# Performance work log

Measured on AMD Instinct MI355X. Metric: run time of the kernel, lower is better.

The kernel has to match this reference:

```python
import jax, jax.numpy as jnp
import numpy as np

B, S, D, H, HD = 1, 4096, 1024, 16, 64
ROPE_THETA = 10000.0


def setup_inputs() -> dict:
    key = jax.random.key(0)
    ks = jax.random.split(key, 10)
    sc = 0.02
    hidden_states = jax.random.normal(ks[0], (B, S, D), dtype=jnp.float32)
    # sorted continuous timestamps in [0, S) (irregularly sampled time series)
    timestamps = jnp.sort(jax.random.uniform(ks[1], (B, S), dtype=jnp.float32), axis=-1) * S
    Wq = jax.random.normal(ks[2], (D, D), dtype=jnp.float32) * sc
    bq = jax.random.normal(ks[3], (D,), dtype=jnp.float32) * sc
    Wk = jax.random.normal(ks[4], (D, D), dtype=jnp.float32) * sc
    bk = jax.random.normal(ks[5], (D,), dtype=jnp.float32) * sc
    Wv = jax.random.normal(ks[6], (D, D), dtype=jnp.float32) * sc
    bv = jax.random.normal(ks[7], (D,), dtype=jnp.float32) * sc
    Wo = jax.random.normal(ks[8], (D, D), dtype=jnp.float32) * sc
    return dict(hidden_states=hidden_states, timestamps=timestamps,
                Wq=Wq, bq=bq, Wk=Wk, bk=bk, Wv=Wv, bv=bv, Wo=Wo)


def _rotate_half(x):
    x1, x2 = jnp.split(x, 2, axis=-1)
    return jnp.concatenate([-x2, x1], axis=-1)


def _ct_rope(q, k, timestamps):
    # q,k: [b,h,s,hd]; timestamps: [b,s] continuous positions
    inv_freq = 1.0 / (ROPE_THETA ** (jnp.arange(0, HD, 2, dtype=jnp.float32) / HD))
    angles = timestamps[:, None, :, None] * inv_freq  # [b,1,s,hd/2]
    angles = jnp.concatenate([angles, angles], axis=-1)  # [b,1,s,hd]
    cos, sin = jnp.cos(angles), jnp.sin(angles)
    q = q * cos + _rotate_half(q) * sin
    k = k * cos + _rotate_half(k) * sin
    return q, k


def reference(hidden_states, timestamps, Wq, bq, Wk, bk, Wv, bv, Wo):
    b, s, _ = hidden_states.shape
    # nn.Linear convention: y = x @ W.T + b
    q = (hidden_states @ Wq.T + bq).reshape(b, s, H, HD).transpose(0, 2, 1, 3)
    k = (hidden_states @ Wk.T + bk).reshape(b, s, H, HD).transpose(0, 2, 1, 3)
    v = (hidden_states @ Wv.T + bv).reshape(b, s, H, HD).transpose(0, 2, 1, 3)
    q, k = _ct_rope(q, k, timestamps)
    scores = jnp.einsum('bhqd,bhkd->bhqk', q, k) / jnp.sqrt(jnp.float32(HD))
    # causal additive mask (built as in HF Qwen2Model)
    causal = jnp.tril(jnp.ones((s, s), dtype=bool))
    neg = jnp.finfo(jnp.float32).min
    scores = jnp.where(causal[None, None], scores, neg)
    attn = jax.nn.softmax(scores.astype(jnp.float32), axis=-1).astype(q.dtype)
    out = jnp.einsum('bhqk,bhkd->bhqd', attn, v)
    out = out.transpose(0, 2, 1, 3).reshape(b, s, H * HD)
    return out @ Wo.T
```

## Files before the change

### kernel.cpp

```cpp
#include <hip/hip_runtime.h>

#define S_LEN  4096
#define DMODEL 1024
#define NHEAD  16
#define HDIM   64

typedef float    f32x4  __attribute__((ext_vector_type(4)));
typedef float    f32x16 __attribute__((ext_vector_type(16)));
typedef _Float16 f16x8  __attribute__((ext_vector_type(8)));
typedef _Float16 f16x4v __attribute__((ext_vector_type(4)));
typedef __fp16   fp16x2 __attribute__((ext_vector_type(2)));
typedef unsigned int u32;
typedef u32 u32x4 __attribute__((ext_vector_type(4)));

__device__ __forceinline__ void gl2lds16(const _Float16* g, _Float16* l) {
  __builtin_amdgcn_global_load_lds(
      (const __attribute__((address_space(1))) unsigned int*)g,
      (__attribute__((address_space(3))) unsigned int*)l, 16, 0, 0);
}

__device__ __forceinline__ u32 pkrtz_u(float a, float b) {
  fp16x2 h = __builtin_amdgcn_cvt_pkrtz(a, b);
  return __builtin_bit_cast(u32, h);
}

__device__ __forceinline__ float m3(float a, float b, float c) {
  return fmaxf(fmaxf(a, b), c);
}

__device__ __forceinline__ float ex2(float x) { return __builtin_amdgcn_exp2f(x); }
__device__ __forceinline__ float lg2(float x) { return __builtin_amdgcn_logf(x); }
__device__ __forceinline__ float rcp(float x) { return __builtin_amdgcn_rcpf(x); }

__global__ void cast_all_k(const float* __restrict__ hs,
                           const float* __restrict__ a, const float* __restrict__ b,
                           const float* __restrict__ c, const float* __restrict__ d,
                           _Float16* __restrict__ ohs,
                           _Float16* __restrict__ oa, _Float16* __restrict__ ob,
                           _Float16* __restrict__ oc, _Float16* __restrict__ od) {
  const int bid = blockIdx.x;
  const float* in;
  _Float16* out;
  int local;
  if (bid < 4096) {
    in = hs; out = ohs; local = bid;
  } else {
    const int seg = (bid - 4096) >> 10;
    local = (bid - 4096) & 1023;
    in  = seg == 0 ? a  : seg == 1 ? b  : seg == 2 ? c  : d;
    out = seg == 0 ? oa : seg == 1 ? ob : seg == 2 ? oc : od;
  }
  const int i = (local * 256 + threadIdx.x) * 4;
  const float4 v = *(const float4*)(in + i);
  f16x4v o = { (_Float16)v.x, (_Float16)v.y, (_Float16)v.z, (_Float16)v.w };
  *(f16x4v*)(out + i) = o;
}

__global__ __launch_bounds__(256)
void gemm_qkv(const _Float16* __restrict__ A,
              const _Float16* __restrict__ Bw,
              const float* __restrict__ bq,
              const float* __restrict__ bk,
              const float* __restrict__ bv,
              const float* __restrict__ ts,
              _Float16* __restrict__ Qb,
              _Float16* __restrict__ Kb,
              _Float16* __restrict__ Vtb)
{
  __shared__ _Float16 lA[128 * 64];
  __shared__ _Float16 lB[128 * 64];

  const int tid  = threadIdx.x;
  const int wid  = tid >> 6;
  const int lane = tid & 63;
  const int l16  = lane & 15;
  const int lg   = lane >> 4;
  const int wr = wid >> 1, wc = wid & 1;
  const int bid = blockIdx.x, xcd = bid & 7, ci = bid >> 3;
  const int n0 = (xcd * 3 + ci / 32) * 128;
  const int m0 = (ci & 31) * 128;
  const int K = DMODEL, M = S_LEN;

  const int lrow   = lane >> 3;
  const int gchunk = (lane & 7) ^ lrow;

  f32x4 acc[4][4] = {};

  for (int k0 = 0; k0 < K; k0 += 64) {
#pragma unroll
    for (int it = 0; it < 4; ++it) {
      const int rbase = (it * 4 + wid) * 8;
      gl2lds16(A  + (size_t)(m0 + rbase + lrow) * K + k0 + gchunk * 8, &lA[rbase * 64]);
      gl2lds16(Bw + (size_t)(n0 + rbase + lrow) * K + k0 + gchunk * 8, &lB[rbase * 64]);
    }
    __syncthreads();
#pragma unroll
    for (int kk = 0; kk < 2; ++kk) {
      f16x8 af[4], bfr[4];
#pragma unroll
      for (int mr = 0; mr < 4; ++mr) {
        const int row = wr * 64 + mr * 16 + l16;
        const int ch  = (kk * 4 + lg) ^ (l16 & 7);
        af[mr] = *(const f16x8*)&lA[row * 64 + ch * 8];
      }
#pragma unroll
      for (int nr = 0; nr < 4; ++nr) {
        const int row = wc * 64 + nr * 16 + l16;
        const int ch  = (kk * 4 + lg) ^ (l16 & 7);
        bfr[nr] = *(const f16x8*)&lB[row * 64 + ch * 8];
      }
#pragma unroll
      for (int mr = 0; mr < 4; ++mr)
#pragma unroll
        for (int nr = 0; nr < 4; ++nr)
          acc[mr][nr] = __builtin_amdgcn_mfma_f32_16x16x32_f16(af[mr], bfr[nr], acc[mr][nr], 0, 0, 0);
    }
    __syncthreads();
  }

  if (n0 >= 2048) {
    const int dbase = n0 - 2048;
    float bvv[4];
#pragma unroll
    for (int nr = 0; nr < 4; ++nr) bvv[nr] = bv[dbase + wc * 64 + nr * 16 + l16];
#pragma unroll
    for (int mr = 0; mr < 4; ++mr) {
      const int mbase = m0 + wr * 64 + mr * 16 + lg * 4;
#pragma unroll
      for (int nr = 0; nr < 4; ++nr) {
        const int d = dbase + wc * 64 + nr * 16 + l16;
        f16x4v o = { (_Float16)(acc[mr][nr][0] + bvv[nr]),
                     (_Float16)(acc[mr][nr][1] + bvv[nr]),
                     (_Float16)(acc[mr][nr][2] + bvv[nr]),
                     (_Float16)(acc[mr][nr][3] + bvv[nr]) };
        *(f16x4v*)&Vtb[(size_t)d * M + mbase] = o;
      }
    }
  } else {
    _Float16* O = (n0 < 1024) ? Qb : Kb;
    const float* bias = (n0 < 1024) ? bq : bk;
    const int nloc = n0 & 1023;
    float bvv[4];
#pragma unroll
    for (int nr = 0; nr < 4; ++nr) bvv[nr] = bias[nloc + wc * 64 + nr * 16 + l16];
    const float L2T  = 13.287712379549449f / 32.0f;
    const float R2PI = 0.15915494309189535f;
    const float inv0 = ex2(-(float)l16 * L2T) * R2PI;
    const float inv1 = ex2(-(float)(l16 + 16) * L2T) * R2PI;
#pragma unroll
    for (int mr = 0; mr < 4; ++mr)
#pragma unroll
      for (int r = 0; r < 4; ++r) {
        const int m = m0 + wr * 64 + mr * 16 + lg * 4 + r;
        const float t = ts[m];
        const float a0 = __builtin_amdgcn_fractf(t * inv0);
        const float a1 = __builtin_amdgcn_fractf(t * inv1);
        const float s0 = __builtin_amdgcn_sinf(a0), c0 = __builtin_amdgcn_cosf(a0);
        const float s1 = __builtin_amdgcn_sinf(a1), c1 = __builtin_amdgcn_cosf(a1);
        const float p0 = acc[mr][0][r] + bvv[0];
        const float p1 = acc[mr][1][r] + bvv[1];
        const float p2 = acc[mr][2][r] + bvv[2];
        const float p3 = acc[mr][3][r] + bvv[3];
        const size_t base = (size_t)m * DMODEL + nloc + wc * 64 + l16;
        O[base + 0 ] = (_Float16)(p0 * c0 - p2 * s0);
        O[base + 16] = (_Float16)(p1 * c1 - p3 * s1);
        O[base + 32] = (_Float16)(p2 * c0 + p0 * s0);
        O[base + 48] = (_Float16)(p3 * c1 + p1 * s1);
      }
  }
}

__global__ __launch_bounds__(256)
void gemm_o(const _Float16* __restrict__ A,
            const _Float16* __restrict__ Bw,
            float* __restrict__ O)
{
  __shared__ _Float16 lA[64 * 64];
  __shared__ _Float16 lB[128 * 64];

  const int tid  = threadIdx.x;
  const int wid  = tid >> 6;
  const int lane = tid & 63;
  const int l16  = lane & 15;
  const int lg   = lane >> 4;
  const int wr = wid >> 1, wc = wid & 1;
  const int bid = blockIdx.x, xcd = bid & 7, ci = bid >> 3;
  const int n0 = xcd * 128;
  const int m0 = ci * 64;
  const int K = DMODEL, N = DMODEL;

  const int lrow   = lane >> 3;
  const int gchunk = (lane & 7) ^ lrow;

  f32x4 acc[2][4] = {};

  for (int k0 = 0; k0 < K; k0 += 64) {
#pragma unroll
    for (int it = 0; it < 2; ++it) {
      const int rbase = (it * 4 + wid) * 8;
      gl2lds16(A + (size_t)(m0 + rbase + lrow) * K + k0 + gchunk * 8, &lA[rbase * 64]);
    }
#pragma unroll
    for (int it = 0; it < 4; ++it) {
      const int rbase = (it * 4 + wid) * 8;
      gl2lds16(Bw + (size_t)(n0 + rbase + lrow) * K + k0 + gchunk * 8, &lB[rbase * 64]);
    }
    __syncthreads();
#pragma unroll
    for (int kk = 0; kk < 2; ++kk) {
      f16x8 af[2], bfr[4];
#pragma unroll
      for (int mr = 0; mr < 2; ++mr) {
        const int row = wr * 32 + mr * 16 + l16;
        const int ch  = (kk * 4 + lg) ^ (l16 & 7);
        af[mr] = *(const f16x8*)&lA[row * 64 + ch * 8];
      }
#pragma unroll
      for (int nr = 0; nr < 4; ++nr) {
        const int row = wc * 64 + nr * 16 + l16;
        const int ch  = (kk * 4 + lg) ^ (l16 & 7);
        bfr[nr] = *(const f16x8*)&lB[row * 64 + ch * 8];
      }
#pragma unroll
      for (int mr = 0; mr < 2; ++mr)
#pragma unroll
        for (int nr = 0; nr < 4; ++nr)
          acc[mr][nr] = __builtin_amdgcn_mfma_f32_16x16x32_f16(af[mr], bfr[nr], acc[mr][nr], 0, 0, 0);
    }
    __syncthreads();
  }

#pragma unroll
  for (int mr = 0; mr < 2; ++mr)
#pragma unroll
    for (int r = 0; r < 4; ++r) {
      const int m = m0 + wr * 32 + mr * 16 + lg * 4 + r;
#pragma unroll
      for (int nr = 0; nr < 4; ++nr) {
        const int n = n0 + wc * 64 + nr * 16 + l16;
        O[(size_t)m * N + n] = acc[mr][nr][r];
      }
    }
}

__device__ __forceinline__ int part_off(int jb) {
  if (jb >= 24) return 40 + (jb - 24) * 4;
  if (jb >= 16) return 16 + (jb - 16) * 3;
  return (jb - 8) * 2;
}

__global__ __launch_bounds__(256, 4)
void attn_fwd(const _Float16* __restrict__ Q,
              const _Float16* __restrict__ Km,
              const _Float16* __restrict__ Vt,
              _Float16* __restrict__ Om,
              _Float16* __restrict__ pO0,
              _Float16* __restrict__ pO1,
              float* __restrict__ ps)
{
  __shared__ __align__(16) _Float16 smem[2 * 2 * 64 * 64];

  const int tid  = threadIdx.x;
  const int wid  = tid >> 6, lane = tid & 63;
  const int l31  = lane & 31;
  const bool hi  = (lane & 32) != 0;
  const int flat = blockIdx.x, xcd = flat & 7, idx = flat >> 3;
  const int h    = xcd * 2 + (idx & 1);
  const int slot = idx >> 1;
  int jb, part, parts;
  if (slot < 32)      { jb = 31 - (slot >> 2);              part = slot & 3;  parts = 4; }
  else if (slot < 56) { const int t = slot - 32; jb = 23 - t / 3; part = t % 3; parts = 3; }
  else if (slot < 72) { const int t = slot - 56; jb = 15 - (t >> 1); part = t & 1; parts = 2; }
  else                { jb = 79 - slot;                     part = 0;        parts = 1; }
  const int nt  = 2 * jb + 2;
  const int kt0 = (nt * part) / parts, kt1 = (nt * (part + 1)) / parts;
  const bool partial = parts > 1;
  const int u = partial ? (h * 72 + part_off(jb) + part) : 0;
  const int q0w = jb * 128 + wid * 32;
  const int sw  = l31 & 7;

  const int rb0  = wid * 16;
  const int rb1  = wid * 16 + 8;
  const int row0 = rb0 + (lane >> 3);
  const int row1 = rb1 + (lane >> 3);
  const int g0   = (lane & 7) ^ (row0 & 7);
  const int g1   = (lane & 7) ^ (row1 & 7);
  const _Float16* kp0 = Km + (size_t)(kt0 * 64 + row0) * DMODEL + h * HDIM + g0 * 8;
  const _Float16* kp1 = Km + (size_t)(kt0 * 64 + row1) * DMODEL + h * HDIM + g1 * 8;
  const _Float16* vp0 = Vt + (size_t)(h * HDIM + row0) * S_LEN + kt0 * 64 + g0 * 8;
  const _Float16* vp1 = Vt + (size_t)(h * HDIM + row1) * S_LEN + kt0 * 64 + g1 * 8;
  const int KSTRIDE = 64 * DMODEL;
  const int VSTRIDE = 64;

  f16x8 qf[4];
  {
    const float qs = 0.18033688f;
    const size_t qbase = (size_t)(q0w + l31) * DMODEL + h * HDIM + (hi ? 8 : 0);
#pragma unroll
    for (int ks = 0; ks < 4; ++ks) {
      f16x8 t = *(const f16x8*)&Q[qbase + ks * 16];
#pragma unroll
      for (int e = 0; e < 8; ++e) qf[ks][e] = (_Float16)((float)t[e] * qs);
    }
  }

  f32x16 acc0, acc1;
#pragma unroll
  for (int r = 0; r < 16; ++r) { acc0[r] = 0.f; acc1[r] = 0.f; }
  float m_run = 0.f, l_run = 0.f;

  gl2lds16(kp0, &smem[rb0 * 64]);
  gl2lds16(kp1, &smem[rb1 * 64]);
  gl2lds16(vp0, &smem[4096 + rb0 * 64]);
  gl2lds16(vp1, &smem[4096 + rb1 * 64]);
  __syncthreads();
  int cur = 0;

  for (int kt = kt0; kt < kt1; ++kt) {
    if (kt + 1 < kt1) {
      kp0 += KSTRIDE; kp1 += KSTRIDE; vp0 += VSTRIDE; vp1 += VSTRIDE;
      const int nb = (cur ^ 1) * 8192;
      gl2lds16(kp0, &smem[nb + rb0 * 64]);
      gl2lds16(kp1, &smem[nb + rb1 * 64]);
      gl2lds16(vp0, &smem[nb + 4096 + rb0 * 64]);
      gl2lds16(vp1, &smem[nb + 4096 + rb1 * 64]);
    }

    const int kv0 = kt * 64;
    if (kv0 <= q0w + 31) {
      const _Float16* kb = &smem[cur * 8192];
      const _Float16* vb = &smem[cur * 8192 + 4096];

      f32x16 s0, s1;
#pragma unroll
      for (int r = 0; r < 16; ++r) { s0[r] = -m_run; s1[r] = -m_run; }
      __builtin_amdgcn_s_setprio(1);
#pragma unroll
      for (int ks = 0; ks < 4; ++ks) {
        const int cs = ((ks * 2 + (hi ? 1 : 0)) ^ sw) * 8;
        const f16x8 ka0 = *(const f16x8*)&kb[l31 * 64 + cs];
        const f16x8 ka1 = *(const f16x8*)&kb[(32 + l31) * 64 + cs];
        s0 = __builtin_amdgcn_mfma_f32_32x32x16_f16(ka0, qf[ks], s0, 0, 0, 0);
        s1 = __builtin_amdgcn_mfma_f32_32x32x16_f16(ka1, qf[ks], s1, 0, 0, 0);
      }
      __builtin_amdgcn_s_setprio(0);

      if (kv0 + 63 > q0w) {
        const int q = q0w + l31;
#pragma unroll
        for (int r = 0; r < 16; ++r) {
          const int kvr = kv0 + (r & 3) + 8 * (r >> 2) + (hi ? 4 : 0);
          if (kvr > q)      s0[r] = -1e30f;
          if (kvr + 32 > q) s1[r] = -1e30f;
        }
      }

      float t10[10];
#pragma unroll
      for (int p = 0; p < 5; ++p) {
        t10[p]     = m3(s0[3*p], s0[3*p+1], s0[3*p+2]);
        t10[5 + p] = m3(s1[3*p], s1[3*p+1], s1[3*p+2]);
      }
      float u0 = m3(t10[0], t10[1], t10[2]);
      float u1 = m3(t10[3], t10[4], s0[15]);
      float u2 = m3(t10[5], t10[6], t10[7]);
      float u3 = m3(t10[8], t10[9], s1[15]);
      float pm = fmaxf(m3(u0, u1, u2), u3);
      pm = fmaxf(pm, __shfl_xor(pm, 32));

      if (!__all(pm <= 10.f)) {
        m_run += pm;
        const float scl = ex2(-pm);
        l_run *= scl;
#pragma unroll
        for (int r = 0; r < 16; ++r) { acc0[r] *= scl; acc1[r] *= scl; }
#pragma unroll
        for (int r = 0; r < 16; ++r) { s0[r] -= pm; s1[r] -= pm; }
      }

      float sa = 0.f, sb = 0.f, sc = 0.f, sd = 0.f;
#pragma unroll
      for (int r = 0; r < 16; r += 2) {
        s0[r]   = ex2(s0[r]);
        s0[r+1] = ex2(s0[r+1]);
        s1[r]   = ex2(s1[r]);
        s1[r+1] = ex2(s1[r+1]);
        sa += s0[r]; sb += s0[r+1]; sc += s1[r]; sd += s1[r+1];
      }
      float rsum = (sa + sb) + (sc + sd);
      rsum += __shfl_xor(rsum, 32);
      l_run += rsum;

      u32 pk[2][8];
#pragma unroll
      for (int p = 0; p < 8; ++p) {
        pk[0][p] = pkrtz_u(s0[2*p], s0[2*p+1]);
        pk[1][p] = pkrtz_u(s1[2*p], s1[2*p+1]);
      }

      __builtin_amdgcn_s_setprio(1);
#pragma unroll
      for (int ks = 0; ks < 4; ++ks) {
        const int c = ks >> 1, base = (ks & 1) * 4;
        auto r0 = __builtin_amdgcn_permlane32_swap((int)pk[c][base + 0], (int)pk[c][base + 2], false, false);
        auto r1 = __builtin_amdgcn_permlane32_swap((int)pk[c][base + 1], (int)pk[c][base + 3], false, false);
        u32x4 bw;
        bw[0] = (u32)r0[0];
        bw[1] = (u32)r1[0];
        bw[2] = (u32)r0[1];
        bw[3] = (u32)r1[1];
        const f16x8 pb = __builtin_bit_cast(f16x8, bw);
        const int cs = ((ks * 2 + (hi ? 1 : 0)) ^ sw) * 8;
        const f16x8 va0 = *(const f16x8*)&vb[l31 * 64 + cs];
        const f16x8 va1 = *(const f16x8*)&vb[(32 + l31) * 64 + cs];
        acc0 = __builtin_amdgcn_mfma_f32_32x32x16_f16(va0, pb, acc0, 0, 0, 0);
        acc1 = __builtin_amdgcn_mfma_f32_32x32x16_f16(va1, pb, acc1, 0, 0, 0);
      }
      __builtin_amdgcn_s_setprio(0);
    }

    __syncthreads();
    cur ^= 1;
  }

  _Float16* tr = &smem[0] + wid * 2304;
  const float invl = rcp(l_run);
#pragma unroll
  for (int r = 0; r < 16; ++r) {
    const int d = (r & 3) + 8 * (r >> 2) + (hi ? 4 : 0);
    tr[l31 * 72 + d]      = (_Float16)(acc0[r] * invl);
    tr[l31 * 72 + 32 + d] = (_Float16)(acc1[r] * invl);
  }
  __syncthreads();
  if (partial) {
    if (!hi) ps[u * 128 + wid * 32 + l31] = m_run + lg2(l_run);
    _Float16* dst = (u < 832) ? (pO0 + (size_t)u * 8192)
                              : (pO1 + (size_t)(u - 832) * 8192);
#pragma unroll
    for (int cc = 0; cc < 4; ++cc) {
      const int qq = cc * 8 + (lane >> 3), c8 = lane & 7;
      const f16x8 v = *(const f16x8*)&tr[qq * 72 + c8 * 8];
      *(f16x8*)&dst[(wid * 32 + qq) * 64 + c8 * 8] = v;
    }
  } else {
#pragma unroll
    for (int cc = 0; cc < 4; ++cc) {
      const int qq = cc * 8 + (lane >> 3), c8 = lane & 7;
      const f16x8 v = *(const f16x8*)&tr[qq * 72 + c8 * 8];
      *(f16x8*)&Om[(size_t)(q0w + qq) * DMODEL + h * HDIM + c8 * 8] = v;
    }
  }
}

__global__ __launch_bounds__(256)
void combine_k(const _Float16* __restrict__ pO0,
               const _Float16* __restrict__ pO1,
               const float* __restrict__ ps,
               _Float16* __restrict__ Om)
{
  const int t  = blockIdx.x * 256 + threadIdx.x;
  const int d8 = t & 7;
  const int hh = (t >> 3) & 15;
  const int q  = 1024 + (t >> 7);
  const int j  = q >> 7;
  const int qr = q & 127;
  const int parts = (j >= 24) ? 4 : (j >= 16) ? 3 : 2;
  const int off   = (j >= 24) ? 40 + (j - 24) * 4
                  : (j >= 16) ? 16 + (j - 16) * 3
                  :             (j - 8) * 2;
  const int u0 = hh * 72 + off;

  float sv[4];
#pragma unroll
  for (int p = 0; p < 4; ++p)
    sv[p] = (p < parts) ? ps[(u0 + p) * 128 + qr] : -1e30f;
  const float S = fmaxf(fmaxf(sv[0], sv[1]), fmaxf(sv[2], sv[3]));

  float o[8] = {0.f, 0.f, 0.f, 0.f, 0.f, 0.f, 0.f, 0.f};
  float tot = 0.f;
#pragma unroll
  for (int p = 0; p < 4; ++p) {
    if (p < parts) {
      const float w = ex2(sv[p] - S);
      tot += w;
      const int uu = u0 + p;
      const _Float16* pp = (uu < 832) ? (pO0 + (size_t)uu * 8192)
                                      : (pO1 + (size_t)(uu - 832) * 8192);
      const f16x8 v = *(const f16x8*)&pp[qr * 64 + d8 * 8];
#pragma unroll
      for (int e = 0; e < 8; ++e) o[e] += w * (float)v[e];
    }
  }
  const float inv = rcp(tot);
  f16x8 ov;
#pragma unroll
  for (int e = 0; e < 8; ++e) ov[e] = (_Float16)(o[e] * inv);
  *(f16x8*)&Om[(size_t)q * DMODEL + hh * 64 + d8 * 8] = ov;
}

extern "C" void kernel_launch(void* const* d_in, const int* in_sizes, int n_in,
                              void* d_out, int out_size, void* d_ws, size_t ws_size,
                              hipStream_t stream)
{
  const float* hs = (const float*)d_in[0];
  const float* ts = (const float*)d_in[1];
  const float* Wq = (const float*)d_in[2];
  const float* bq = (const float*)d_in[3];
  const float* Wk = (const float*)d_in[4];
  const float* bk = (const float*)d_in[5];
  const float* Wv = (const float*)d_in[6];
  const float* bv = (const float*)d_in[7];
  const float* Wo = (const float*)d_in[8];
  float* out = (float*)d_out;

  char* ws = (char*)d_ws;
  const size_t MB = 1024 * 1024;
  _Float16* hsb  = (_Float16*)(ws + 0 * MB);
  _Float16* wqb  = (_Float16*)(ws + 8 * MB);
  _Float16* wkb  = (_Float16*)(ws + 10 * MB);
  _Float16* wvb  = (_Float16*)(ws + 12 * MB);
  _Float16* wob  = (_Float16*)(ws + 14 * MB);
  _Float16* Qb   = (_Float16*)(ws + 16 * MB);
  _Float16* Kb   = (_Float16*)(ws + 24 * MB);
  _Float16* Vtb  = (_Float16*)(ws + 32 * MB);
  _Float16* attb = (_Float16*)(ws + 40 * MB);
  _Float16* pO0  = (_Float16*)(ws + 0 * MB);
  _Float16* pO1  = (_Float16*)d_out;
  float*    ps   = (float*)   (ws + (size_t)13631488);

  cast_all_k<<<dim3(8192), dim3(256), 0, stream>>>(hs, Wq, Wk, Wv, Wo,
                                                   hsb, wqb, wkb, wvb, wob);

  gemm_qkv<<<dim3(768), dim3(256), 0, stream>>>(
      hsb, wqb, bq, bk, bv, ts, Qb, Kb, Vtb);

  attn_fwd<<<dim3(1280), dim3(256), 0, stream>>>(Qb, Kb, Vtb, attb, pO0, pO1, ps);
  combine_k<<<dim3(1536), dim3(256), 0, stream>>>(pO0, pO1, ps, attb);

  gemm_o<<<dim3(512), dim3(256), 0, stream>>>(attb, wob, out);
}
```

Baseline: 136.2 us.

## Software-pipeline QK^T one tile ahead of softmax and PV in attention loop

Restructures the attention main loop so the QK^T MFMA for tile k is issued while the softmax and PV MFMA for tile k-1 run, letting matrix and vector work overlap. K gets a double buffer and V a triple buffer in LDS (5 tiles instead of 4), and the running-max offset baked into the early scores is corrected with a delta when the max changes. The cost is more LDS per block, which may lower occupancy, plus extra registers for the in-flight score tiles.

```diff
diff --git a/kernel.cpp b/kernel.cpp
--- a/kernel.cpp
+++ b/kernel.cpp
@@ -258,7 +258,7 @@
               _Float16* __restrict__ pO1,
               float* __restrict__ ps)
 {
-  __shared__ __align__(16) _Float16 smem[2 * 2 * 64 * 64];
+  __shared__ __align__(16) _Float16 smem[5 * 4096];
 
   const int tid  = threadIdx.x;
   const int wid  = tid >> 6, lane = tid & 63;
@@ -307,64 +307,112 @@
   f32x16 acc0, acc1;
 #pragma unroll
   for (int r = 0; r < 16; ++r) { acc0[r] = 0.f; acc1[r] = 0.f; }
-  float m_run = 0.f, l_run = 0.f;
-
-  gl2lds16(kp0, &smem[rb0 * 64]);
-  gl2lds16(kp1, &smem[rb1 * 64]);
-  gl2lds16(vp0, &smem[4096 + rb0 * 64]);
-  gl2lds16(vp1, &smem[4096 + rb1 * 64]);
+  float m_run = 0.f, l_run = 0.f, m_bake = 0.f;
+
+  {
+    const int vb = 8192 + (kt0 % 3) * 4096;
+    gl2lds16(kp0, &smem[rb0 * 64]);
+    gl2lds16(kp1, &smem[rb1 * 64]);
+    gl2lds16(vp0, &smem[vb + rb0 * 64]);
+    gl2lds16(vp1, &smem[vb + rb1 * 64]);
+  }
   __syncthreads();
-  int cur = 0;
-
-  for (int kt = kt0; kt < kt1; ++kt) {
-    if (kt + 1 < kt1) {
+
+  f32x16 sp0, sp1;
+  {
+#pragma unroll
+    for (int r = 0; r < 16; ++r) { sp0[r] = 0.f; sp1[r] = 0.f; }
+    const _Float16* kb = &smem[0];
+    __builtin_amdgcn_s_setprio(1);
+#pragma unroll
+    for (int ks = 0; ks < 4; ++ks) {
+      const int cs = ((ks * 2 + (hi ? 1 : 0)) ^ sw) * 8;
+      const f16x8 ka0 = *(const f16x8*)&kb[l31 * 64 + cs];
+      const f16x8 ka1 = *(const f16x8*)&kb[(32 + l31) * 64 + cs];
+      sp0 = __builtin_amdgcn_mfma_f32_32x32x16_f16(ka0, qf[ks], sp0, 0, 0, 0);
+      sp1 = __builtin_amdgcn_mfma_f32_32x32x16_f16(ka1, qf[ks], sp1, 0, 0, 0);
+    }
+    __builtin_amdgcn_s_setprio(0);
+    if (kt0 * 64 + 63 > q0w) {
+      const int q = q0w + l31;
+#pragma unroll
+      for (int r = 0; r < 16; ++r) {
+        const int kvr = kt0 * 64 + (r & 3) + 8 * (r >> 2) + (hi ? 4 : 0);
+        if (kvr > q)      sp0[r] = -1e30f;
+        if (kvr + 32 > q) sp1[r] = -1e30f;
+      }
+    }
+  }
+  if (kt0 + 1 < kt1) {
+    kp0 += KSTRIDE; kp1 += KSTRIDE; vp0 += VSTRIDE; vp1 += VSTRIDE;
+    const int vb = 8192 + ((kt0 + 1) % 3) * 4096;
+    gl2lds16(kp0, &smem[4096 + rb0 * 64]);
+    gl2lds16(kp1, &smem[4096 + rb1 * 64]);
+    gl2lds16(vp0, &smem[vb + rb0 * 64]);
+    gl2lds16(vp1, &smem[vb + rb1 * 64]);
+  }
+
+  int kc = 1;
+  int vprev = kt0 % 3;
+  int vnext = (kt0 + 2) % 3;
+
+  for (int k = kt0 + 1; k <= kt1; ++k) {
+    __syncthreads();
+
+    if (k + 1 < kt1) {
       kp0 += KSTRIDE; kp1 += KSTRIDE; vp0 += VSTRIDE; vp1 += VSTRIDE;
-      const int nb = (cur ^ 1) * 8192;
-      gl2lds16(kp0, &smem[nb + rb0 * 64]);
-      gl2lds16(kp1, &smem[nb + rb1 * 64]);
-      gl2lds16(vp0, &smem[nb + 4096 + rb0 * 64]);
-      gl2lds16(vp1, &smem[nb + 4096 + rb1 * 64]);
-    }
-
-    const int kv0 = kt * 64;
-    if (kv0 <= q0w + 31) {
-      const _Float16* kb = &smem[cur * 8192];
-      const _Float16* vb = &smem[cur * 8192 + 4096];
-
-      f32x16 s0, s1;
-#pragma unroll
-      for (int r = 0; r < 16; ++r) { s0[r] = -m_run; s1[r] = -m_run; }
+      const int kb_off = (kc ^ 1) * 4096;
+      const int vb_off = 8192 + vnext * 4096;
+      gl2lds16(kp0, &smem[kb_off + rb0 * 64]);
+      gl2lds16(kp1, &smem[kb_off + rb1 * 64]);
+      gl2lds16(vp0, &smem[vb_off + rb0 * 64]);
+      gl2lds16(vp1, &smem[vb_off + rb1 * 64]);
+    }
+
+    f32x16 sn0, sn1;
+    float m_bake_new = m_run;
+    const bool act_k = (k < kt1) && (k * 64 <= q0w + 31);
+    if (act_k) {
+#pragma unroll
+      for (int r = 0; r < 16; ++r) { sn0[r] = -m_run; sn1[r] = -m_run; }
+      const _Float16* kb = &smem[kc * 4096];
       __builtin_amdgcn_s_setprio(1);
 #pragma unroll
       for (int ks = 0; ks < 4; ++ks) {
         const int cs = ((ks * 2 + (hi ? 1 : 0)) ^ sw) * 8;
         const f16x8 ka0 = *(const f16x8*)&kb[l31 * 64 + cs];
         const f16x8 ka1 = *(const f16x8*)&kb[(32 + l31) * 64 + cs];
-        s0 = __builtin_amdgcn_mfma_f32_32x32x16_f16(ka0, qf[ks], s0, 0, 0, 0);
-        s1 = __builtin_amdgcn_mfma_f32_32x32x16_f16(ka1, qf[ks], s1, 0, 0, 0);
+        sn0 = __builtin_amdgcn_mfma_f32_32x32x16_f16(ka0, qf[ks], sn0, 0, 0, 0);
+        sn1 = __builtin_amdgcn_mfma_f32_32x32x16_f16(ka1, qf[ks], sn1, 0, 0, 0);
       }
       __builtin_amdgcn_s_setprio(0);
-
-      if (kv0 + 63 > q0w) {
+      if (k * 64 + 63 > q0w) {
         const int q = q0w + l31;
 #pragma unroll
         for (int r = 0; r < 16; ++r) {
-          const int kvr = kv0 + (r & 3) + 8 * (r >> 2) + (hi ? 4 : 0);
-          if (kvr > q)      s0[r] = -1e30f;
-          if (kvr + 32 > q) s1[r] = -1e30f;
+          const int kvr = k * 64 + (r & 3) + 8 * (r >> 2) + (hi ? 4 : 0);
+          if (kvr > q)      sn0[r] = -1e30f;
+          if (kvr + 32 > q) sn1[r] = -1e30f;
         }
       }
-
+    }
+
+    if ((k - 1) * 64 <= q0w + 31) {
+      const float delta = m_run - m_bake;
+      if (delta != 0.f) {
+#pragma unroll
+        for (int r = 0; r < 16; ++r) { sp0[r] -= delta; sp1[r] -= delta; }
+      }
       float t10[10];
 #pragma unroll
       for (int p = 0; p < 5; ++p) {
-        t10[p]     = m3(s0[3*p], s0[3*p+1], s0[3*p+2]);
-        t10[5 + p] = m3(s1[3*p], s1[3*p+1], s1[3*p+2]);
+        t10[p]     = m3(sp0[3*p], sp0[3*p+1], sp0[3*p+2]);
+        t10[5 + p] = m3(sp1[3*p], sp1[3*p+1], sp1[3*p+2]);
       }
       float u0 = m3(t10[0], t10[1], t10[2]);
-      float u1 = m3(t10[3], t10[4], s0[15]);
+      float u1 = m3(t10[3], t10[4], sp0[15]);
       float u2 = m3(t10[5], t10[6], t10[7]);
-      float u3 = m3(t10[8], t10[9], s1[15]);
+      float u3 = m3(t10[8], t10[9], sp1[15]);
       float pm = fmaxf(m3(u0, u1, u2), u3);
       pm = fmaxf(pm, __shfl_xor(pm, 32));
 
@@ -375,17 +423,17 @@
 #pragma unroll
         for (int r = 0; r < 16; ++r) { acc0[r] *= scl; acc1[r] *= scl; }
 #pragma unroll
-        for (int r = 0; r < 16; ++r) { s0[r] -= pm; s1[r] -= pm; }
+        for (int r = 0; r < 16; ++r) { sp0[r] -= pm; sp1[r] -= pm; }
       }
 
       float sa = 0.f, sb = 0.f, sc = 0.f, sd = 0.f;
 #pragma unroll
       for (int r = 0; r < 16; r += 2) {
-        s0[r]   = ex2(s0[r]);
-        s0[r+1] = ex2(s0[r+1]);
-        s1[r]   = ex2(s1[r]);
-        s1[r+1] = ex2(s1[r+1]);
-        sa += s0[r]; sb += s0[r+1]; sc += s1[r]; sd += s1[r+1];
+        sp0[r]   = ex2(sp0[r]);
+        sp0[r+1] = ex2(sp0[r+1]);
+        sp1[r]   = ex2(sp1[r]);
+        sp1[r+1] = ex2(sp1[r+1]);
+        sa += sp0[r]; sb += sp0[r+1]; sc += sp1[r]; sd += sp1[r+1];
       }
       float rsum = (sa + sb) + (sc + sd);
       rsum += __shfl_xor(rsum, 32);
@@ -394,10 +442,11 @@
       u32 pk[2][8];
 #pragma unroll
       for (int p = 0; p < 8; ++p) {
-        pk[0][p] = pkrtz_u(s0[2*p], s0[2*p+1]);
-        pk[1][p] = pkrtz_u(s1[2*p], s1[2*p+1]);
-      }
-
+        pk[0][p] = pkrtz_u(sp0[2*p], sp0[2*p+1]);
+        pk[1][p] = pkrtz_u(sp1[2*p], sp1[2*p+1]);
+      }
+
+      const _Float16* vb = &smem[8192 + vprev * 4096];
       __builtin_amdgcn_s_setprio(1);
 #pragma unroll
       for (int ks = 0; ks < 4; ++ks) {
@@ -419,10 +468,14 @@
       __builtin_amdgcn_s_setprio(0);
     }
 
-    __syncthreads();
-    cur ^= 1;
-  }
-
+    if (act_k) { sp0 = sn0; sp1 = sn1; m_bake = m_bake_new; }
+
+    kc ^= 1;
+    vprev = (vprev == 2) ? 0 : vprev + 1;
+    vnext = (vnext == 2) ? 0 : vnext + 1;
+  }
+
+  __syncthreads();
   _Float16* tr = &smem[0] + wid * 2304;
   const float invl = rcp(l_run);
 #pragma unroll
```

After: 202.8 us. 48.9% more time.
